# Performance work log

Hardware: AMD Instinct MI355X
Metric: run time of the kernel (lower is better)

The kernel has to match this reference:

```python
import jax, jax.numpy as jnp
import numpy as np

V, R, A, C, T = 50000, 5, 8, 32, 32  # vertices, radial, angular, in-channels, templates
DELTA = 2                             # rotation_delta -> n_rotations = A // DELTA = 4


def setup_inputs() -> dict:
    key = jax.random.key(0)
    ks = jax.random.split(key, 6)
    signal = jax.random.normal(ks[0], (V, C), jnp.float32)
    bc_idx = jax.random.randint(ks[1], (V, R, A, 3), 0, V, dtype=jnp.int32)
    w = jax.random.uniform(ks[2], (V, R, A, 3), jnp.float32)
    bc_w = w / jnp.sum(w, axis=-1, keepdims=True)  # barycentric weights sum to 1
    templ1 = jax.random.normal(ks[3], (T, R, A, C), jnp.float32) * 0.05
    bias1 = jnp.zeros((T,), jnp.float32)
    templ2 = jax.random.normal(ks[4], (T, R, A, T), jnp.float32) * 0.05
    bias2 = jnp.zeros((T,), jnp.float32)
    return {"signal": signal, "bc_idx": bc_idx, "bc_w": bc_w,
            "templ1": templ1, "bias1": bias1, "templ2": templ2, "bias2": bias2}


def _conv_dirac(x, bc_idx, bc_w, templ, bias):
    """Dirac intrinsic surface convolution.
    x: [V, Cin]; bc_idx/bc_w: [V, R, A, 3]; templ: [T, R, A, Cin] -> [V, n_rot, T]."""
    # Barycentric interpolation of the mesh signal at template vertices.
    gathered = x[bc_idx]                                   # [V, R, A, 3, Cin]
    interp = jnp.einsum('vrai,vraic->vrac', bc_w, gathered)  # [V, R, A, Cin]
    n_rot = A // DELTA
    # Rotating the patch by +s angular steps == correlating with templ rolled by +s.
    rot_t = jnp.stack([jnp.roll(templ, r * DELTA, axis=2) for r in range(n_rot)])  # [n_rot, T, R, A, Cin]
    return jnp.einsum('vrac,ntrac->vnt', interp, rot_t) + bias  # [V, n_rot, T]


def _amp(x):
    # AngularMaxPooling: max over the rotation axis.
    return jnp.max(x, axis=1)


def reference(signal, bc_idx, bc_w, templ1, bias1, templ2, bias2):
    s = jax.nn.relu(_conv_dirac(signal, bc_idx, bc_w, templ1, bias1))  # conv1 (relu)
    s = _amp(s)                                                        # [V, T]
    s = _conv_dirac(s, bc_idx, bc_w, templ2, bias2)                    # conv2 (linear)
    s = _amp(s)                                                        # [V, T]
    # input_dim == amt_templates -> no rescale branch; residual add + output relu
    return jax.nn.relu(s + signal)
```

## Files before the change

### kernel.cpp

```cpp
#include <hip/hip_runtime.h>
#include <hip/hip_bf16.h>

#define VN 50000
#define RN 5
#define AN 8
#define CN 32
#define TN 32
#define KSTEPS 40
#define NB 8

typedef __attribute__((ext_vector_type(8))) short bf16x8;
typedef __attribute__((ext_vector_type(4))) float f32x4;

__device__ __forceinline__ float b2f(short s) {
    union { unsigned u; float f; } cv;
    cv.u = ((unsigned)(unsigned short)s) << 16;
    return cv.f;
}
__device__ __forceinline__ short f2b(float f) {
    union { float f; unsigned u; } cv; cv.f = f;
    unsigned r = cv.u + 0x7fff + ((cv.u >> 16) & 1);
    return (short)(r >> 16);
}

__global__ void pack_x(const float* __restrict__ x, __hip_bfloat16* __restrict__ xb, int n4) {
    int i = blockIdx.x * blockDim.x + threadIdx.x;
    if (i >= n4) return;
    float4 v = ((const float4*)x)[i];
    ushort4 o;
    o.x = (unsigned short)f2b(v.x);
    o.y = (unsigned short)f2b(v.y);
    o.z = (unsigned short)f2b(v.z);
    o.w = (unsigned short)f2b(v.w);
    ((ushort4*)xb)[i] = o;
}

__global__ void build_Bp(const float* __restrict__ t1, const float* __restrict__ t2,
                         __hip_bfloat16* __restrict__ B1, __hip_bfloat16* __restrict__ B2) {
    int m = blockIdx.x * blockDim.x + threadIdx.x;
    if (m >= KSTEPS * NB * 64 * 8) return;
    int j = m & 7;
    int lane = (m >> 3) & 63;
    int nb = (m >> 9) & 7;
    int kstep = m >> 12;
    int c = ((lane >> 4) << 3) + j;
    int r = kstep >> 3, a = kstep & 7;
    int nt = nb * 16 + (lane & 15);
    int n = nt >> 5, t = nt & 31;
    int asrc = (a - 2 * n + 8) & 7;
    int src = ((t * RN + r) * AN + asrc) * CN + c;
    B1[m] = __hip_bfloat16(); ((unsigned short*)B1)[m] = (unsigned short)f2b(t1[src]);
    ((unsigned short*)B2)[m] = (unsigned short)f2b(t2[src]);
}

__device__ __forceinline__ bf16x8 gather_blend(const __hip_bfloat16* __restrict__ xb,
                                               const int* __restrict__ ip,
                                               const float* __restrict__ wp, int c0) {
    int i0 = ip[0], i1 = ip[1], i2 = ip[2];
    float w0 = wp[0], w1 = wp[1], w2 = wp[2];
    bf16x8 g0 = *(const bf16x8*)((const unsigned short*)xb + i0 * CN + c0);
    bf16x8 g1 = *(const bf16x8*)((const unsigned short*)xb + i1 * CN + c0);
    bf16x8 g2 = *(const bf16x8*)((const unsigned short*)xb + i2 * CN + c0);
    bf16x8 o;
#pragma unroll
    for (int j = 0; j < 8; ++j) {
        float f = fmaf(w0, b2f(g0[j]), fmaf(w1, b2f(g1[j]), w2 * b2f(g2[j])));
        o[j] = f2b(f);
    }
    return o;
}

template<bool FIRST>
__global__ __launch_bounds__(128)
void conv_mfma(const __hip_bfloat16* __restrict__ xb,
               const int*   __restrict__ bc_idx,
               const float* __restrict__ bc_w,
               const __hip_bfloat16* __restrict__ Bp,
               const float* __restrict__ bias,
               const float* __restrict__ signal,
               __hip_bfloat16* __restrict__ out_bf,
               float* __restrict__ out_f)
{
    const int tid = threadIdx.x;
    const int wid = tid >> 6;
    const int lane = tid & 63;
    const int vbase = (blockIdx.x * 2 + wid) * 32;

    const int arow = lane & 15;
    const int c0 = (lane >> 4) << 3;

    int v0 = vbase + arow;
    int v1 = v0 + 16;
    int vc0 = v0 < VN ? v0 : VN - 1;
    int vc1 = v1 < VN ? v1 : VN - 1;

    const int* ip0 = bc_idx + vc0 * 120;
    const int* ip1 = bc_idx + vc1 * 120;
    const float* wp0 = bc_w + vc0 * 120;
    const float* wp1 = bc_w + vc1 * 120;
    const bf16x8* Bfrag = (const bf16x8*)Bp + lane;

    f32x4 acc[2][NB];
#pragma unroll
    for (int mi = 0; mi < 2; ++mi)
#pragma unroll
        for (int nb = 0; nb < NB; ++nb) acc[mi][nb] = (f32x4)(0.f);

#pragma unroll 2
    for (int ks = 0; ks < KSTEPS; ++ks) {
        bf16x8 afrag0 = gather_blend(xb, ip0, wp0, c0);
        bf16x8 afrag1 = gather_blend(xb, ip1, wp1, c0);
        ip0 += 3; ip1 += 3; wp0 += 3; wp1 += 3;
#pragma unroll
        for (int nb = 0; nb < NB; ++nb) {
            bf16x8 bfrag = Bfrag[(ks * NB + nb) * 64];
            acc[0][nb] = __builtin_amdgcn_mfma_f32_16x16x32_bf16(afrag0, bfrag, acc[0][nb], 0, 0, 0);
            acc[1][nb] = __builtin_amdgcn_mfma_f32_16x16x32_bf16(afrag1, bfrag, acc[1][nb], 0, 0, 0);
        }
    }

    const int colD = lane & 15;
    const int rbase = (lane >> 4) << 2;
#pragma unroll
    for (int mi = 0; mi < 2; ++mi) {
#pragma unroll
        for (int q = 0; q < 2; ++q) {
            f32x4 mx;
#pragma unroll
            for (int rg = 0; rg < 4; ++rg)
                mx[rg] = fmaxf(fmaxf(acc[mi][q][rg], acc[mi][q + 2][rg]),
                               fmaxf(acc[mi][q + 4][rg], acc[mi][q + 6][rg]));
            int t = q * 16 + colD;
            float b = bias[t];
#pragma unroll
            for (int rg = 0; rg < 4; ++rg) {
                int v = vbase + mi * 16 + rbase + rg;
                if (v < VN) {
                    float val = mx[rg] + b;
                    if (FIRST) {
                        ((unsigned short*)out_bf)[v * CN + t] =
                            (unsigned short)f2b(fmaxf(val, 0.f));
                    } else {
                        val += signal[v * CN + t];
                        out_f[v * CN + t] = fmaxf(val, 0.f);
                    }
                }
            }
        }
    }
}

extern "C" void kernel_launch(void* const* d_in, const int* in_sizes, int n_in,
                              void* d_out, int out_size, void* d_ws, size_t ws_size,
                              hipStream_t stream) {
    const float* signal = (const float*)d_in[0];
    const int*   bc_idx = (const int*)d_in[1];
    const float* bc_w   = (const float*)d_in[2];
    const float* t1     = (const float*)d_in[3];
    const float* b1     = (const float*)d_in[4];
    const float* t2     = (const float*)d_in[5];
    const float* b2     = (const float*)d_in[6];
    float* out = (float*)d_out;

    __hip_bfloat16* ws = (__hip_bfloat16*)d_ws;
    __hip_bfloat16* xb  = ws;
    __hip_bfloat16* s1  = ws + VN * CN;
    __hip_bfloat16* Bp1 = ws + 2 * VN * CN;
    __hip_bfloat16* Bp2 = Bp1 + KSTEPS * NB * 64 * 8;

    pack_x<<<(VN * CN / 4 + 255) / 256, 256, 0, stream>>>(signal, xb, VN * CN / 4);
    build_Bp<<<(KSTEPS * NB * 64 * 8) / 256, 256, 0, stream>>>(t1, t2, Bp1, Bp2);

    int blocks = (VN + 63) / 64;
    conv_mfma<true ><<<blocks, 128, 0, stream>>>(xb, bc_idx, bc_w, Bp1, b1, nullptr, s1, nullptr);
    conv_mfma<false><<<blocks, 128, 0, stream>>>(s1, bc_idx, bc_w, Bp2, b2, signal, nullptr, out);
}
```

Before: 221.5 us.

## Use one 16-row tile per wave, vectorize barycentric loads, raise occupancy

Each wave now handles 16 vertices instead of 32, with four waves per 256-thread block, halving the accumulator registers and letting launch bounds request more resident waves. Barycentric indices and weights for a radial ring are fetched as 128-bit nontemporal vector loads instead of scalar loads, and the output and residual signal use nontemporal accesses. The intent is more latency hiding for the random gathers. The cost is that each B fragment is loaded from memory twice as often per vertex, and the 24-entry index/weight arrays may add register pressure.

```diff
diff --git a/kernel.cpp b/kernel.cpp
--- a/kernel.cpp
+++ b/kernel.cpp
@@ -5,12 +5,12 @@
 #define RN 5
 #define AN 8
 #define CN 32
-#define TN 32
 #define KSTEPS 40
 #define NB 8
 
 typedef __attribute__((ext_vector_type(8))) short bf16x8;
 typedef __attribute__((ext_vector_type(4))) float f32x4;
+typedef __attribute__((ext_vector_type(4))) int   i32x4;
 
 __device__ __forceinline__ float b2f(short s) {
     union { unsigned u; float f; } cv;
@@ -49,29 +49,12 @@
     int n = nt >> 5, t = nt & 31;
     int asrc = (a - 2 * n + 8) & 7;
     int src = ((t * RN + r) * AN + asrc) * CN + c;
-    B1[m] = __hip_bfloat16(); ((unsigned short*)B1)[m] = (unsigned short)f2b(t1[src]);
+    ((unsigned short*)B1)[m] = (unsigned short)f2b(t1[src]);
     ((unsigned short*)B2)[m] = (unsigned short)f2b(t2[src]);
 }
 
-__device__ __forceinline__ bf16x8 gather_blend(const __hip_bfloat16* __restrict__ xb,
-                                               const int* __restrict__ ip,
-                                               const float* __restrict__ wp, int c0) {
-    int i0 = ip[0], i1 = ip[1], i2 = ip[2];
-    float w0 = wp[0], w1 = wp[1], w2 = wp[2];
-    bf16x8 g0 = *(const bf16x8*)((const unsigned short*)xb + i0 * CN + c0);
-    bf16x8 g1 = *(const bf16x8*)((const unsigned short*)xb + i1 * CN + c0);
-    bf16x8 g2 = *(const bf16x8*)((const unsigned short*)xb + i2 * CN + c0);
-    bf16x8 o;
-#pragma unroll
-    for (int j = 0; j < 8; ++j) {
-        float f = fmaf(w0, b2f(g0[j]), fmaf(w1, b2f(g1[j]), w2 * b2f(g2[j])));
-        o[j] = f2b(f);
-    }
-    return o;
-}
-
 template<bool FIRST>
-__global__ __launch_bounds__(128)
+__global__ __launch_bounds__(256, 3)
 void conv_mfma(const __hip_bfloat16* __restrict__ xb,
                const int*   __restrict__ bc_idx,
                const float* __restrict__ bc_w,
@@ -84,66 +67,79 @@
     const int tid = threadIdx.x;
     const int wid = tid >> 6;
     const int lane = tid & 63;
-    const int vbase = (blockIdx.x * 2 + wid) * 32;
+    const int vbase = blockIdx.x * 64 + wid * 16;
 
     const int arow = lane & 15;
     const int c0 = (lane >> 4) << 3;
 
-    int v0 = vbase + arow;
-    int v1 = v0 + 16;
-    int vc0 = v0 < VN ? v0 : VN - 1;
-    int vc1 = v1 < VN ? v1 : VN - 1;
+    int v = vbase + arow;
+    int vc = v < VN ? v : VN - 1;
 
-    const int* ip0 = bc_idx + vc0 * 120;
-    const int* ip1 = bc_idx + vc1 * 120;
-    const float* wp0 = bc_w + vc0 * 120;
-    const float* wp1 = bc_w + vc1 * 120;
+    const i32x4* ipb = (const i32x4*)(bc_idx + vc * 120);
+    const f32x4* wpb = (const f32x4*)(bc_w  + vc * 120);
+    const unsigned short* xs = (const unsigned short*)xb;
     const bf16x8* Bfrag = (const bf16x8*)Bp + lane;
 
-    f32x4 acc[2][NB];
+    f32x4 acc[NB];
 #pragma unroll
-    for (int mi = 0; mi < 2; ++mi)
+    for (int nb = 0; nb < NB; ++nb) acc[nb] = (f32x4)(0.f);
+
+    for (int r = 0; r < RN; ++r) {
+        int I[24]; float W[24];
 #pragma unroll
-        for (int nb = 0; nb < NB; ++nb) acc[mi][nb] = (f32x4)(0.f);
-
-#pragma unroll 2
-    for (int ks = 0; ks < KSTEPS; ++ks) {
-        bf16x8 afrag0 = gather_blend(xb, ip0, wp0, c0);
-        bf16x8 afrag1 = gather_blend(xb, ip1, wp1, c0);
-        ip0 += 3; ip1 += 3; wp0 += 3; wp1 += 3;
+        for (int q = 0; q < 6; ++q) {
+            i32x4 iv = __builtin_nontemporal_load(ipb + r * 6 + q);
+            f32x4 wv = __builtin_nontemporal_load(wpb + r * 6 + q);
+            I[q * 4 + 0] = iv[0]; I[q * 4 + 1] = iv[1];
+            I[q * 4 + 2] = iv[2]; I[q * 4 + 3] = iv[3];
+            W[q * 4 + 0] = wv[0]; W[q * 4 + 1] = wv[1];
+            W[q * 4 + 2] = wv[2]; W[q * 4 + 3] = wv[3];
+        }
 #pragma unroll
-        for (int nb = 0; nb < NB; ++nb) {
-            bf16x8 bfrag = Bfrag[(ks * NB + nb) * 64];
-            acc[0][nb] = __builtin_amdgcn_mfma_f32_16x16x32_bf16(afrag0, bfrag, acc[0][nb], 0, 0, 0);
-            acc[1][nb] = __builtin_amdgcn_mfma_f32_16x16x32_bf16(afrag1, bfrag, acc[1][nb], 0, 0, 0);
+        for (int a = 0; a < AN; ++a) {
+            const int e = a * 3;
+            int   i0 = I[e], i1 = I[e + 1], i2 = I[e + 2];
+            float w0 = W[e], w1 = W[e + 1], w2 = W[e + 2];
+            bf16x8 g0 = *(const bf16x8*)(xs + (size_t)i0 * CN + c0);
+            bf16x8 g1 = *(const bf16x8*)(xs + (size_t)i1 * CN + c0);
+            bf16x8 g2 = *(const bf16x8*)(xs + (size_t)i2 * CN + c0);
+            bf16x8 af;
+#pragma unroll
+            for (int j = 0; j < 8; ++j) {
+                float f = fmaf(w0, b2f(g0[j]), fmaf(w1, b2f(g1[j]), w2 * b2f(g2[j])));
+                af[j] = f2b(f);
+            }
+            const int ks = r * AN + a;
+#pragma unroll
+            for (int nb = 0; nb < NB; ++nb) {
+                bf16x8 bfr = Bfrag[(ks * NB + nb) * 64];
+                acc[nb] = __builtin_amdgcn_mfma_f32_16x16x32_bf16(af, bfr, acc[nb], 0, 0, 0);
+            }
         }
     }
 
     const int colD = lane & 15;
     const int rbase = (lane >> 4) << 2;
 #pragma unroll
-    for (int mi = 0; mi < 2; ++mi) {
+    for (int q = 0; q < 2; ++q) {
+        f32x4 mx;
 #pragma unroll
-        for (int q = 0; q < 2; ++q) {
-            f32x4 mx;
+        for (int rg = 0; rg < 4; ++rg)
+            mx[rg] = fmaxf(fmaxf(acc[q][rg], acc[q + 2][rg]),
+                           fmaxf(acc[q + 4][rg], acc[q + 6][rg]));
+        int t = q * 16 + colD;
+        float b = bias[t];
 #pragma unroll
-            for (int rg = 0; rg < 4; ++rg)
-                mx[rg] = fmaxf(fmaxf(acc[mi][q][rg], acc[mi][q + 2][rg]),
-                               fmaxf(acc[mi][q + 4][rg], acc[mi][q + 6][rg]));
-            int t = q * 16 + colD;
-            float b = bias[t];
-#pragma unroll
-            for (int rg = 0; rg < 4; ++rg) {
-                int v = vbase + mi * 16 + rbase + rg;
-                if (v < VN) {
-                    float val = mx[rg] + b;
-                    if (FIRST) {
-                        ((unsigned short*)out_bf)[v * CN + t] =
-                            (unsigned short)f2b(fmaxf(val, 0.f));
-                    } else {
-                        val += signal[v * CN + t];
-                        out_f[v * CN + t] = fmaxf(val, 0.f);
-                    }
+        for (int rg = 0; rg < 4; ++rg) {
+            int vv = vbase + rbase + rg;
+            if (vv < VN) {
+                float val = mx[rg] + b;
+                if (FIRST) {
+                    ((unsigned short*)out_bf)[vv * CN + t] =
+                        (unsigned short)f2b(fmaxf(val, 0.f));
+                } else {
+                    val += __builtin_nontemporal_load(signal + vv * CN + t);
+                    __builtin_nontemporal_store(fmaxf(val, 0.f), out_f + vv * CN + t);
                 }
             }
         }
@@ -172,6 +168,6 @@
     build_Bp<<<(KSTEPS * NB * 64 * 8) / 256, 256, 0, stream>>>(t1, t2, Bp1, Bp2);
 
     int blocks = (VN + 63) / 64;
-    conv_mfma<true ><<<blocks, 128, 0, stream>>>(xb, bc_idx, bc_w, Bp1, b1, nullptr, s1, nullptr);
-    conv_mfma<false><<<blocks, 128, 0, stream>>>(s1, bc_idx, bc_w, Bp2, b2, signal, nullptr, out);
+    conv_mfma<true ><<<blocks, 256, 0, stream>>>(xb, bc_idx, bc_w, Bp1, b1, nullptr, s1, nullptr);
+    conv_mfma<false><<<blocks, 256, 0, stream>>>(s1, bc_idx, bc_w, Bp2, b2, signal, nullptr, out);
 }
```

After: 305.9 us. 1.38x slower.
